# Kernel tuning notes

Measured on AMD Instinct MI355X. Metric: run time of the kernel, lower is better.

Reference implementation:

```python
import jax, jax.numpy as jnp
import numpy as np

DIM = 2048
NUM_HEADS = 16
NUM_KV_HEADS = 4
HEAD_DIM = DIM // NUM_HEADS  # 128
ROPE_DIMS = HEAD_DIM         # rope_dims=0 -> full head_dim
ROPE_BASE = 10000.0
EPS = jnp.finfo(jnp.float32).eps  # torch F.rms_norm default eps


def _rms_norm(x):
    # F.rms_norm over last dim, no learned weight
    return x * jax.lax.rsqrt(jnp.mean(x * x, axis=-1, keepdims=True) + EPS)


def _rope_cos_sin(seq_len, dtype):
    inv_freq = 1.0 / (ROPE_BASE ** (jnp.arange(0, ROPE_DIMS, 2, dtype=jnp.float32) / ROPE_DIMS))
    t = jnp.arange(seq_len, dtype=jnp.float32)
    freqs = jnp.outer(t, inv_freq)  # [S, rope_dims/2]
    return jnp.cos(freqs).astype(dtype), jnp.sin(freqs).astype(dtype)


def _apply_rotary(x, cos, sin):
    # x: [B, H, S, hd]; cos/sin: [S, rope_dims/2] broadcast over B,H
    half = ROPE_DIMS // 2
    x1, x2 = x[..., :half], x[..., half:ROPE_DIMS]
    x_pass = x[..., ROPE_DIMS:]
    rotated = jnp.concatenate((x1 * cos + x2 * sin, -x1 * sin + x2 * cos), axis=-1)
    return jnp.concatenate((rotated, x_pass), axis=-1) if x_pass.shape[-1] else rotated


def setup_inputs() -> dict:
    key = jax.random.key(0)
    ks = jax.random.split(key, 6)
    B, S = 2, 2048
    kv_dim = NUM_KV_HEADS * HEAD_DIM
    scale = 0.02
    return {
        "x": jax.random.normal(ks[0], (B, S, DIM), dtype=jnp.float32),
        "Wq": jax.random.normal(ks[1], (DIM, DIM), dtype=jnp.float32) * scale,
        "Wk": jax.random.normal(ks[2], (kv_dim, DIM), dtype=jnp.float32) * scale,
        "Wv": jax.random.normal(ks[3], (kv_dim, DIM), dtype=jnp.float32) * scale,
        "Wproj": jax.random.normal(ks[4], (DIM, DIM), dtype=jnp.float32) * scale,
        "q_gain": jnp.full((NUM_HEADS,), 1.0, dtype=jnp.float32),
    }


def reference(x, Wq, Wk, Wv, Wproj, q_gain):
    B, S, D = x.shape
    H, KV, hd = NUM_HEADS, NUM_KV_HEADS, HEAD_DIM
    group = H // KV

    # QKV projections (Linear: y = x @ W.T)
    q = (x @ Wq.T).reshape(B, S, H, hd).transpose(0, 2, 1, 3)    # [B,H,S,hd]
    k = (x @ Wk.T).reshape(B, S, KV, hd).transpose(0, 2, 1, 3)   # [B,KV,S,hd]
    v = (x @ Wv.T).reshape(B, S, KV, hd).transpose(0, 2, 1, 3)

    # Per-head RMSNorm on q/k
    q = _rms_norm(q)
    k = _rms_norm(k)

    # RoPE
    cos, sin = _rope_cos_sin(S, q.dtype)
    q = _apply_rotary(q, cos, sin)
    k = _apply_rotary(k, cos, sin)

    # Per-head gain on q
    q = q * q_gain[None, :, None, None]

    # GQA: expand kv heads to H
    k = jnp.repeat(k, group, axis=1)  # [B,H,S,hd]
    v = jnp.repeat(v, group, axis=1)

    # Causal SDPA
    sm_scale = 1.0 / np.sqrt(hd)
    scores = jnp.einsum('bhqd,bhkd->bhqk', q, k) * sm_scale
    causal = jnp.tril(jnp.ones((S, S), dtype=bool))
    scores = jnp.where(causal, scores, -jnp.inf)
    attn = jax.nn.softmax(scores, axis=-1)
    y = jnp.einsum('bhqk,bhkd->bhqd', attn, v)

    y = y.transpose(0, 2, 1, 3).reshape(B, S, D)
    return y @ Wproj.T
```

## Files before the change

### kernel.cpp

```cpp
#include <hip/hip_runtime.h>
#include <hip/hip_bf16.h>
#include <stdint.h>

namespace {

constexpr int kB = 2;
constexpr int kS = 2048;
constexpr int kD = 2048;
constexpr int kH = 16;
constexpr int kKV = 4;
constexpr int kHd = 128;
constexpr int kM = kB * kS;
constexpr int kQKN = kD + kKV * kHd;

using bf = __bf16;
typedef bf bf16x8 __attribute__((ext_vector_type(8)));
typedef float f32x4 __attribute__((ext_vector_type(4)));

__device__ __forceinline__ f32x4 mfma16(bf16x8 a, bf16x8 b, f32x4 c) {
  return __builtin_amdgcn_mfma_f32_16x16x32_bf16(a, b, c, 0, 0, 0);
}

__device__ __forceinline__ void gload_lds16(const bf* g, bf* l) {
  __builtin_amdgcn_global_load_lds(
      (const __attribute__((address_space(1))) void*)(uintptr_t)g,
      (__attribute__((address_space(3))) void*)l, 16, 0, 0);
}

__global__ __launch_bounds__(256) void cvt_kernel(const float* __restrict__ src,
                                                  bf* __restrict__ dst, int n4) {
  int i = blockIdx.x * 256 + threadIdx.x;
  if (i >= n4) return;
  float4 v = reinterpret_cast<const float4*>(src)[i];
  union { bf h[4]; uint2 u; } o;
  o.h[0] = (bf)v.x; o.h[1] = (bf)v.y; o.h[2] = (bf)v.z; o.h[3] = (bf)v.w;
  reinterpret_cast<uint2*>(dst)[i] = o.u;
}

template <typename CT>
__global__ __launch_bounds__(256) void gemm_bt(const bf* __restrict__ A, int lda,
                                               const bf* __restrict__ Bm, int ldb,
                                               CT* __restrict__ C, int ldc, int K) {
  __shared__ bf As[128 * 64];
  __shared__ bf Bs[128 * 64];
  const int tid = threadIdx.x;
  const int w = tid >> 6, lane = tid & 63;
  const int r16 = lane & 15, kg = lane >> 4;
  const int bm = blockIdx.y * 128, bn = blockIdx.x * 128;
  const int wy = (w >> 1) * 64, wx = (w & 1) * 64;
  f32x4 acc[4][4] = {};
  for (int kt = 0; kt < K; kt += 64) {
    __syncthreads();
#pragma unroll
    for (int r = 0; r < 4; r++) {
      int u = r * 256 + tid;
      int row = u >> 3;
      int cb = ((u & 7) * 16) ^ ((row & 7) << 4);
      gload_lds16(A + (size_t)(bm + row) * lda + kt + (cb >> 1),
                  As + (size_t)(r * 256 + w * 64) * 8);
      gload_lds16(Bm + (size_t)(bn + row) * ldb + kt + (cb >> 1),
                  Bs + (size_t)(r * 256 + w * 64) * 8);
    }
    __syncthreads();
#pragma unroll
    for (int ks = 0; ks < 2; ks++) {
      bf16x8 af[4], bfr[4];
#pragma unroll
      for (int m = 0; m < 4; m++) {
        int row = wy + m * 16 + r16;
        af[m] = *reinterpret_cast<const bf16x8*>(
            reinterpret_cast<const char*>(As) + row * 128 +
            ((ks * 64 + kg * 16) ^ ((row & 7) << 4)));
      }
#pragma unroll
      for (int n = 0; n < 4; n++) {
        int row = wx + n * 16 + r16;
        bfr[n] = *reinterpret_cast<const bf16x8*>(
            reinterpret_cast<const char*>(Bs) + row * 128 +
            ((ks * 64 + kg * 16) ^ ((row & 7) << 4)));
      }
#pragma unroll
      for (int m = 0; m < 4; m++)
#pragma unroll
        for (int n = 0; n < 4; n++)
          acc[m][n] = mfma16(af[m], bfr[n], acc[m][n]);
    }
  }
#pragma unroll
  for (int m = 0; m < 4; m++)
#pragma unroll
    for (int n = 0; n < 4; n++)
#pragma unroll
      for (int r = 0; r < 4; r++) {
        int row = bm + wy + m * 16 + kg * 4 + r;
        int col = bn + wx + n * 16 + r16;
        C[(size_t)row * ldc + col] = (CT)acc[m][n][r];
      }
}

__global__ __launch_bounds__(256) void normrope(bf* __restrict__ qk,
                                                const float* __restrict__ qgain) {
  const int tid = threadIdx.x;
  const int w = tid >> 6, lane = tid & 63;
  int v = blockIdx.x * 4 + w;
  int b = v / (kS * (kH + kKV));
  int rem = v % (kS * (kH + kKV));
  int s = rem / (kH + kKV);
  int j = rem % (kH + kKV);
  int colbase = (j < kH) ? j * kHd : kD + (j - kH) * kHd;
  size_t base = (size_t)(b * kS + s) * kQKN + colbase;
  float e1 = (float)qk[base + lane];
  float e2 = (float)qk[base + 64 + lane];
  float ss = e1 * e1 + e2 * e2;
#pragma unroll
  for (int m = 1; m < 64; m <<= 1) ss += __shfl_xor(ss, m);
  float inv = rsqrtf(ss * (1.0f / 128.0f) + 1.1920929e-7f);
  e1 *= inv; e2 *= inv;
  float invfreq = powf(10000.0f, -(float)lane * (1.0f / 64.0f));
  float ang = (float)s * invfreq;
  float sn, cs;
  sincosf(ang, &sn, &cs);
  float o1 = e1 * cs + e2 * sn;
  float o2 = -e1 * sn + e2 * cs;
  if (j < kH) {
    float g = qgain[j] * (0.08838834764831845f * 1.4426950408889634f);
    o1 *= g; o2 *= g;
  }
  qk[base + lane] = (bf)o1;
  qk[base + 64 + lane] = (bf)o2;
}

__global__ __launch_bounds__(256) void attn_kernel(const bf* __restrict__ qk,
                                                   const bf* __restrict__ vt,
                                                   bf* __restrict__ y) {
  __shared__ bf Ks[2][64 * 128];
  __shared__ bf Vs[2][128 * 64];
  __shared__ bf Ps[4][16 * 64];
  const int tid = threadIdx.x;
  const int w = tid >> 6, lane = tid & 63;
  const int r16 = lane & 15, kg = lane >> 4;
  const int pairIdx = blockIdx.x;
  const int bh = blockIdx.y;
  const int b = bh >> 4, h = bh & 15, kvh = h >> 2;
  const size_t rowbase = (size_t)b * kS;
  const bf* kbase = qk + kD + kvh * kHd;
  const bf* vbase = vt + (size_t)(kvh * kHd) * kM + b * kS;

  auto stage = [&](int buf, int kt) {
#pragma unroll
    for (int r = 0; r < 4; r++) {
      int u = r * 256 + tid;
      int krow = u >> 4;
      int cb = ((u & 15) * 16) ^ ((krow & 7) << 4);
      gload_lds16(kbase + (rowbase + kt * 64 + krow) * kQKN + (cb >> 1),
                  Ks[buf] + (size_t)(r * 256 + w * 64) * 8);
    }
#pragma unroll
    for (int r = 0; r < 4; r++) {
      int u = r * 256 + tid;
      int vrow = u >> 3;
      int cb = ((u & 7) * 16) ^ ((vrow & 7) << 4);
      gload_lds16(vbase + (size_t)vrow * kM + kt * 64 + (cb >> 1),
                  Vs[buf] + (size_t)(r * 256 + w * 64) * 8);
    }
  };

#pragma unroll 1
  for (int ph = 0; ph < 2; ph++) {
    const int qi = ph ? (31 - pairIdx) : pairIdx;
    const int q0 = qi * 64;
    const int qw = q0 + w * 16;
    const int qrow = qw + r16;

    bf16x8 qf[4];
#pragma unroll
    for (int ks = 0; ks < 4; ks++) {
      qf[ks] = *reinterpret_cast<const bf16x8*>(
          qk + (rowbase + qrow) * kQKN + h * kHd + ks * 32 + kg * 8);
    }

    f32x4 o[8] = {};
    float mrun = -1e30f, lrun = 0.f;

    __syncthreads();
    int cur = 0;
    stage(0, 0);

    for (int kt = 0; kt <= qi; kt++) {
      __syncthreads();
      if (kt < qi) stage(cur ^ 1, kt + 1);

      f32x4 sf[4];
      __builtin_amdgcn_s_setprio(1);
#pragma unroll
      for (int n = 0; n < 4; n++) {
        bf16x8 kf[4];
#pragma unroll
        for (int ks = 0; ks < 4; ks++) {
          int krow = n * 16 + r16;
          kf[ks] = *reinterpret_cast<const bf16x8*>(
              reinterpret_cast<const char*>(Ks[cur]) + krow * 256 +
              ((ks * 64 + kg * 16) ^ ((krow & 7) << 4)));
        }
        f32x4 a = {};
#pragma unroll
        for (int ks = 0; ks < 4; ks++) a = mfma16(kf[ks], qf[ks], a);
        sf[n] = a;
      }
      __builtin_amdgcn_s_setprio(0);

      if (kt * 64 + 63 > qw) {
#pragma unroll
        for (int n = 0; n < 4; n++)
#pragma unroll
          for (int r = 0; r < 4; r++) {
            int col = kt * 64 + n * 16 + kg * 4 + r;
            sf[n][r] = (col <= qrow) ? sf[n][r] : -1e30f;
          }
      }

      float rmax = sf[0][0];
#pragma unroll
      for (int n = 0; n < 4; n++)
#pragma unroll
        for (int r = 0; r < 4; r++) rmax = fmaxf(rmax, sf[n][r]);
      rmax = fmaxf(rmax, __shfl_xor(rmax, 16));
      rmax = fmaxf(rmax, __shfl_xor(rmax, 32));

      if (!__all(rmax <= mrun + 8.0f)) {
        float mnew = fmaxf(mrun, rmax);
        float resc = exp2f(mrun - mnew);
        mrun = mnew;
        lrun *= resc;
        float rq[4];
#pragma unroll
        for (int r = 0; r < 4; r++) rq[r] = __shfl(resc, kg * 4 + r);
#pragma unroll
        for (int nf = 0; nf < 8; nf++)
#pragma unroll
          for (int r = 0; r < 4; r++) o[nf][r] *= rq[r];
      }

      float rsum = 0.f;
#pragma unroll
      for (int n = 0; n < 4; n++)
#pragma unroll
        for (int r = 0; r < 4; r++) {
          float p = exp2f(sf[n][r] - mrun);
          sf[n][r] = p;
          rsum += p;
        }
      rsum += __shfl_xor(rsum, 16);
      rsum += __shfl_xor(rsum, 32);
      lrun += rsum;

      {
        char* prow = reinterpret_cast<char*>(Ps[w]) + r16 * 128;
#pragma unroll
        for (int n = 0; n < 4; n++) {
          union { bf h[4]; uint2 u2; } pk;
          pk.h[0] = (bf)sf[n][0]; pk.h[1] = (bf)sf[n][1];
          pk.h[2] = (bf)sf[n][2]; pk.h[3] = (bf)sf[n][3];
          *reinterpret_cast<uint2*>(prow + ((n * 32 + kg * 8) ^ ((r16 & 7) << 4))) = pk.u2;
        }
      }
      asm volatile("s_waitcnt lgkmcnt(0)" ::: "memory");
      __builtin_amdgcn_sched_barrier(0);

      const bf* pw2 = Ps[w];
      __builtin_amdgcn_s_setprio(1);
#pragma unroll
      for (int ksv = 0; ksv < 2; ksv++) {
        bf16x8 pa = *reinterpret_cast<const bf16x8*>(
            reinterpret_cast<const char*>(pw2) + r16 * 128 +
            ((ksv * 64 + kg * 16) ^ ((r16 & 7) << 4)));
#pragma unroll
        for (int nf = 0; nf < 8; nf++) {
          int vrow = nf * 16 + r16;
          bf16x8 vb = *reinterpret_cast<const bf16x8*>(
              reinterpret_cast<const char*>(Vs[cur]) + vrow * 128 +
              ((ksv * 64 + kg * 16) ^ ((vrow & 7) << 4)));
          o[nf] = mfma16(pa, vb, o[nf]);
        }
      }
      __builtin_amdgcn_s_setprio(0);
      cur ^= 1;
    }

    float linv = 1.0f / lrun;
    float lq[4];
#pragma unroll
    for (int r = 0; r < 4; r++) lq[r] = __shfl(linv, kg * 4 + r);
#pragma unroll
    for (int nf = 0; nf < 8; nf++)
#pragma unroll
      for (int r = 0; r < 4; r++) {
        int s = q0 + w * 16 + kg * 4 + r;
        int d = nf * 16 + r16;
        y[(rowbase + s) * kD + h * kHd + d] = (bf)(o[nf][r] * lq[r]);
      }
  }
}

}

extern "C" void kernel_launch(void* const* d_in, const int* in_sizes, int n_in,
                              void* d_out, int out_size, void* d_ws, size_t ws_size,
                              hipStream_t stream) {
  const float* x  = (const float*)d_in[0];
  const float* Wq = (const float*)d_in[1];
  const float* Wk = (const float*)d_in[2];
  const float* Wv = (const float*)d_in[3];
  const float* Wp = (const float*)d_in[4];
  const float* qg = (const float*)d_in[5];

  bf* xb    = (bf*)d_ws;
  bf* wqkvb = xb + (size_t)kM * kD;
  bf* wpb   = wqkvb + (size_t)3072 * kD;
  bf* qkbuf = wpb + (size_t)kD * kD;
  bf* vtbuf = qkbuf + (size_t)kM * kQKN;
  bf* yb    = vtbuf + (size_t)512 * kM;

  cvt_kernel<<<(kM * kD / 4) / 256, 256, 0, stream>>>(x, xb, kM * kD / 4);
  cvt_kernel<<<(kD * kD / 4) / 256, 256, 0, stream>>>(Wq, wqkvb, kD * kD / 4);
  cvt_kernel<<<(512 * kD / 4) / 256, 256, 0, stream>>>(Wk, wqkvb + (size_t)kD * kD, 512 * kD / 4);
  cvt_kernel<<<(512 * kD / 4) / 256, 256, 0, stream>>>(Wv, wqkvb + (size_t)kD * kD + (size_t)512 * kD, 512 * kD / 4);
  cvt_kernel<<<(kD * kD / 4) / 256, 256, 0, stream>>>(Wp, wpb, kD * kD / 4);

  gemm_bt<bf><<<dim3(kQKN / 128, kM / 128), 256, 0, stream>>>(xb, kD, wqkvb, kD, qkbuf, kQKN, kD);

  gemm_bt<bf><<<dim3(kM / 128, 512 / 128), 256, 0, stream>>>(
      wqkvb + (size_t)(kD + 512) * kD, kD, xb, kD, vtbuf, kM, kD);

  normrope<<<(kB * kS * (kH + kKV)) / 4, 256, 0, stream>>>(qkbuf, qg);

  attn_kernel<<<dim3(16, kB * kH), 256, 0, stream>>>(qkbuf, vtbuf, yb);

  gemm_bt<float><<<dim3(kD / 128, kM / 128), 256, 0, stream>>>(yb, kD, wpb, kD, (float*)d_out, kD, kD);
}
```

Before: 262.5 us.

## Rewrite attention with 32x32 MFMA, 128-row query tiles, register-resident P

New measurement: 261.8 us. About the same (-0.3%).

```diff
diff --git a/kernel.cpp b/kernel.cpp
--- a/kernel.cpp
+++ b/kernel.cpp
@@ -16,9 +16,13 @@
 using bf = __bf16;
 typedef bf bf16x8 __attribute__((ext_vector_type(8)));
 typedef float f32x4 __attribute__((ext_vector_type(4)));
+typedef float f32x16 __attribute__((ext_vector_type(16)));
 
 __device__ __forceinline__ f32x4 mfma16(bf16x8 a, bf16x8 b, f32x4 c) {
   return __builtin_amdgcn_mfma_f32_16x16x32_bf16(a, b, c, 0, 0, 0);
+}
+__device__ __forceinline__ f32x16 mfma32(bf16x8 a, bf16x8 b, f32x16 c) {
+  return __builtin_amdgcn_mfma_f32_32x32x16_bf16(a, b, c, 0, 0, 0);
 }
 
 __device__ __forceinline__ void gload_lds16(const bf* g, bf* l) {
@@ -130,17 +134,17 @@
   qk[base + 64 + lane] = (bf)o2;
 }
 
-__global__ __launch_bounds__(256) void attn_kernel(const bf* __restrict__ qk,
-                                                   const bf* __restrict__ vt,
-                                                   bf* __restrict__ y) {
+__global__ __launch_bounds__(256, 2) void attn_kernel(const bf* __restrict__ qk,
+                                                      const bf* __restrict__ vt,
+                                                      bf* __restrict__ y) {
   __shared__ bf Ks[2][64 * 128];
   __shared__ bf Vs[2][128 * 64];
-  __shared__ bf Ps[4][16 * 64];
   const int tid = threadIdx.x;
   const int w = tid >> 6, lane = tid & 63;
-  const int r16 = lane & 15, kg = lane >> 4;
-  const int pairIdx = blockIdx.x;
-  const int bh = blockIdx.y;
+  const int q32 = lane & 31, hi = lane >> 5;
+  const int bh = blockIdx.x;
+  const int jb = blockIdx.y;
+  const int qi = (jb < 8) ? jb : 23 - jb;
   const int b = bh >> 4, h = bh & 15, kvh = h >> 2;
   const size_t rowbase = (size_t)b * kS;
   const bf* kbase = qk + kD + kvh * kHd;
@@ -165,66 +169,60 @@
     }
   };
 
-#pragma unroll 1
-  for (int ph = 0; ph < 2; ph++) {
-    const int qi = ph ? (31 - pairIdx) : pairIdx;
-    const int q0 = qi * 64;
-    const int qw = q0 + w * 16;
-    const int qrow = qw + r16;
-
-    bf16x8 qf[4];
-#pragma unroll
-    for (int ks = 0; ks < 4; ks++) {
-      qf[ks] = *reinterpret_cast<const bf16x8*>(
-          qk + (rowbase + qrow) * kQKN + h * kHd + ks * 32 + kg * 8);
-    }
-
-    f32x4 o[8] = {};
-    float mrun = -1e30f, lrun = 0.f;
-
+  const int q0 = qi * 128;
+  const int qg0 = q0 + w * 32;
+  const int qrow = qg0 + q32;
+
+  bf16x8 qf[8];
+#pragma unroll
+  for (int dc = 0; dc < 8; dc++)
+    qf[dc] = *reinterpret_cast<const bf16x8*>(
+        qk + (rowbase + qrow) * kQKN + h * kHd + dc * 16 + hi * 8);
+
+  f32x16 o[4] = {};
+  float mrun = -1e30f, lrun = 0.f;
+
+  int cur = 0;
+  stage(0, 0);
+  const int ntiles = 2 * qi + 2;
+
+  for (int kt = 0; kt < ntiles; kt++) {
     __syncthreads();
-    int cur = 0;
-    stage(0, 0);
-
-    for (int kt = 0; kt <= qi; kt++) {
-      __syncthreads();
-      if (kt < qi) stage(cur ^ 1, kt + 1);
-
-      f32x4 sf[4];
+    if (kt + 1 < ntiles) stage(cur ^ 1, kt + 1);
+
+    if (kt * 64 <= qg0 + 31) {
+      f32x16 sf[2];
       __builtin_amdgcn_s_setprio(1);
 #pragma unroll
-      for (int n = 0; n < 4; n++) {
-        bf16x8 kf[4];
-#pragma unroll
-        for (int ks = 0; ks < 4; ks++) {
-          int krow = n * 16 + r16;
-          kf[ks] = *reinterpret_cast<const bf16x8*>(
+      for (int kb = 0; kb < 2; kb++) {
+        f32x16 a = {};
+#pragma unroll
+        for (int dc = 0; dc < 8; dc++) {
+          int krow = kb * 32 + q32;
+          bf16x8 kf = *reinterpret_cast<const bf16x8*>(
               reinterpret_cast<const char*>(Ks[cur]) + krow * 256 +
-              ((ks * 64 + kg * 16) ^ ((krow & 7) << 4)));
+              ((dc * 32 + hi * 16) ^ ((krow & 7) << 4)));
+          a = mfma32(kf, qf[dc], a);
         }
-        f32x4 a = {};
-#pragma unroll
-        for (int ks = 0; ks < 4; ks++) a = mfma16(kf[ks], qf[ks], a);
-        sf[n] = a;
+        sf[kb] = a;
       }
       __builtin_amdgcn_s_setprio(0);
 
-      if (kt * 64 + 63 > qw) {
-#pragma unroll
-        for (int n = 0; n < 4; n++)
-#pragma unroll
-          for (int r = 0; r < 4; r++) {
-            int col = kt * 64 + n * 16 + kg * 4 + r;
-            sf[n][r] = (col <= qrow) ? sf[n][r] : -1e30f;
+      if (kt * 64 + 63 > qg0) {
+#pragma unroll
+        for (int kb = 0; kb < 2; kb++)
+#pragma unroll
+          for (int r = 0; r < 16; r++) {
+            int kgl = kt * 64 + kb * 32 + (r & 3) + 8 * (r >> 2) + 4 * hi;
+            sf[kb][r] = (kgl <= qrow) ? sf[kb][r] : -1e30f;
           }
       }
 
       float rmax = sf[0][0];
 #pragma unroll
-      for (int n = 0; n < 4; n++)
-#pragma unroll
-        for (int r = 0; r < 4; r++) rmax = fmaxf(rmax, sf[n][r]);
-      rmax = fmaxf(rmax, __shfl_xor(rmax, 16));
+      for (int kb = 0; kb < 2; kb++)
+#pragma unroll
+        for (int r = 0; r < 16; r++) rmax = fmaxf(rmax, sf[kb][r]);
       rmax = fmaxf(rmax, __shfl_xor(rmax, 32));
 
       if (!__all(rmax <= mrun + 8.0f)) {
@@ -232,74 +230,79 @@
         float resc = exp2f(mrun - mnew);
         mrun = mnew;
         lrun *= resc;
-        float rq[4];
-#pragma unroll
-        for (int r = 0; r < 4; r++) rq[r] = __shfl(resc, kg * 4 + r);
-#pragma unroll
-        for (int nf = 0; nf < 8; nf++)
-#pragma unroll
-          for (int r = 0; r < 4; r++) o[nf][r] *= rq[r];
+        float rq[16];
+#pragma unroll
+        for (int r = 0; r < 16; r++)
+          rq[r] = __shfl(resc, (r & 3) + 8 * (r >> 2) + 4 * hi);
+#pragma unroll
+        for (int db = 0; db < 4; db++)
+#pragma unroll
+          for (int r = 0; r < 16; r++) o[db][r] *= rq[r];
       }
 
       float rsum = 0.f;
 #pragma unroll
-      for (int n = 0; n < 4; n++)
-#pragma unroll
-        for (int r = 0; r < 4; r++) {
-          float p = exp2f(sf[n][r] - mrun);
-          sf[n][r] = p;
+      for (int kb = 0; kb < 2; kb++)
+#pragma unroll
+        for (int r = 0; r < 16; r++) {
+          float p = exp2f(sf[kb][r] - mrun);
+          sf[kb][r] = p;
           rsum += p;
         }
-      rsum += __shfl_xor(rsum, 16);
       rsum += __shfl_xor(rsum, 32);
       lrun += rsum;
 
-      {
-        char* prow = reinterpret_cast<char*>(Ps[w]) + r16 * 128;
-#pragma unroll
-        for (int n = 0; n < 4; n++) {
-          union { bf h[4]; uint2 u2; } pk;
-          pk.h[0] = (bf)sf[n][0]; pk.h[1] = (bf)sf[n][1];
-          pk.h[2] = (bf)sf[n][2]; pk.h[3] = (bf)sf[n][3];
-          *reinterpret_cast<uint2*>(prow + ((n * 32 + kg * 8) ^ ((r16 & 7) << 4))) = pk.u2;
+      bf16x8 pa[4];
+#pragma unroll
+      for (int kb = 0; kb < 2; kb++) {
+        uint32_t wa[4], wb[4];
+#pragma unroll
+        for (int g = 0; g < 4; g++) {
+          asm("v_cvt_pk_bf16_f32 %0, %1, %2"
+              : "=v"(wa[g]) : "v"(sf[kb][4 * g + 0]), "v"(sf[kb][4 * g + 1]));
+          asm("v_cvt_pk_bf16_f32 %0, %1, %2"
+              : "=v"(wb[g]) : "v"(sf[kb][4 * g + 2]), "v"(sf[kb][4 * g + 3]));
         }
-      }
-      asm volatile("s_waitcnt lgkmcnt(0)" ::: "memory");
-      __builtin_amdgcn_sched_barrier(0);
-
-      const bf* pw2 = Ps[w];
+        asm volatile("v_permlane32_swap_b32 %0, %1" : "+v"(wa[0]), "+v"(wa[1]));
+        asm volatile("v_permlane32_swap_b32 %0, %1" : "+v"(wb[0]), "+v"(wb[1]));
+        asm volatile("v_permlane32_swap_b32 %0, %1" : "+v"(wa[2]), "+v"(wa[3]));
+        asm volatile("v_permlane32_swap_b32 %0, %1" : "+v"(wb[2]), "+v"(wb[3]));
+        union { uint32_t u[4]; bf16x8 v; } p0, p1;
+        p0.u[0] = wa[0]; p0.u[1] = wb[0]; p0.u[2] = wa[1]; p0.u[3] = wb[1];
+        p1.u[0] = wa[2]; p1.u[1] = wb[2]; p1.u[2] = wa[3]; p1.u[3] = wb[3];
+        pa[2 * kb + 0] = p0.v;
+        pa[2 * kb + 1] = p1.v;
+      }
+
       __builtin_amdgcn_s_setprio(1);
 #pragma unroll
-      for (int ksv = 0; ksv < 2; ksv++) {
-        bf16x8 pa = *reinterpret_cast<const bf16x8*>(
-            reinterpret_cast<const char*>(pw2) + r16 * 128 +
-            ((ksv * 64 + kg * 16) ^ ((r16 & 7) << 4)));
-#pragma unroll
-        for (int nf = 0; nf < 8; nf++) {
-          int vrow = nf * 16 + r16;
+      for (int c = 0; c < 4; c++)
+#pragma unroll
+        for (int db = 0; db < 4; db++) {
+          int vrow = db * 32 + q32;
           bf16x8 vb = *reinterpret_cast<const bf16x8*>(
               reinterpret_cast<const char*>(Vs[cur]) + vrow * 128 +
-              ((ksv * 64 + kg * 16) ^ ((vrow & 7) << 4)));
-          o[nf] = mfma16(pa, vb, o[nf]);
+              ((c * 32 + hi * 16) ^ ((vrow & 7) << 4)));
+          o[db] = mfma32(pa[c], vb, o[db]);
         }
-      }
       __builtin_amdgcn_s_setprio(0);
-      cur ^= 1;
-    }
-
-    float linv = 1.0f / lrun;
-    float lq[4];
-#pragma unroll
-    for (int r = 0; r < 4; r++) lq[r] = __shfl(linv, kg * 4 + r);
-#pragma unroll
-    for (int nf = 0; nf < 8; nf++)
-#pragma unroll
-      for (int r = 0; r < 4; r++) {
-        int s = q0 + w * 16 + kg * 4 + r;
-        int d = nf * 16 + r16;
-        y[(rowbase + s) * kD + h * kHd + d] = (bf)(o[nf][r] * lq[r]);
-      }
+    }
+    cur ^= 1;
   }
+
+  float linv = 1.0f / lrun;
+  float lq[16];
+#pragma unroll
+  for (int r = 0; r < 16; r++)
+    lq[r] = __shfl(linv, (r & 3) + 8 * (r >> 2) + 4 * hi);
+#pragma unroll
+  for (int db = 0; db < 4; db++)
+#pragma unroll
+    for (int r = 0; r < 16; r++) {
+      int s = qg0 + (r & 3) + 8 * (r >> 2) + 4 * hi;
+      int d = db * 32 + q32;
+      y[(rowbase + s) * kD + h * kHd + d] = (bf)(o[db][r] * lq[r]);
+    }
 }
 
 }
@@ -334,7 +337,7 @@
 
   normrope<<<(kB * kS * (kH + kKV)) / 4, 256, 0, stream>>>(qkbuf, qg);
 
-  attn_kernel<<<dim3(16, kB * kH), 256, 0, stream>>>(qkbuf, vtbuf, yb);
+  attn_kernel<<<dim3(kB * kH, 16), 256, 0, stream>>>(qkbuf, vtbuf, yb);
 
   gemm_bt<float><<<dim3(kD / 128, kM / 128), 256, 0, stream>>>(yb, kD, wpb, kD, (float*)d_out, kD, kD);
 }
```
